# Kernel tuning notes

Measured on AMD Instinct MI355X. Metric: run time of the kernel, lower is better.

## Reference

```python
import jax, jax.numpy as jnp
import numpy as np

COMMITMENT_COST = 0.25
K, D = 1024, 64          # num_embeddings, embedding_dim
B, T = 32, 4096          # batch, tokens per batch element


def setup_inputs() -> dict:
    key = jax.random.key(0)
    k1, k2 = jax.random.split(key)
    inputs = jax.random.normal(k1, (B, T, D), dtype=jnp.float32)
    # xavier_uniform over [K, D]: bound = sqrt(6/(K+D))
    bound = float(np.sqrt(6.0 / (K + D)))
    embedding = jax.random.uniform(k2, (K, D), dtype=jnp.float32,
                                   minval=-bound, maxval=bound)
    return {"inputs": inputs, "embedding": embedding}


def reference(inputs, embedding):
    input_shape = inputs.shape
    flat = inputs.reshape(-1, embedding.shape[1])            # [N, D]
    input_sq = jnp.sum(flat ** 2, axis=1, keepdims=True)     # [N, 1]
    embed_sq = jnp.sum(embedding ** 2, axis=1)               # [K]
    dot = flat @ embedding.T                                 # [N, K]
    distances = input_sq + embed_sq - 2.0 * dot              # [N, K]
    idx = jnp.argmin(distances, axis=1)                      # [N]
    quant = embedding[idx]                                   # [N, D]
    q_latent_loss = jnp.mean((quant - jax.lax.stop_gradient(flat)) ** 2)
    e_latent_loss = jnp.mean((jax.lax.stop_gradient(quant) - flat) ** 2)
    loss = q_latent_loss + COMMITMENT_COST * e_latent_loss
    # straight-through estimator
    quant_st = flat + jax.lax.stop_gradient(quant - flat)
    quant_st = quant_st.reshape(input_shape)
    encoding_indices = idx.reshape(input_shape[0], -1)
    return quant_st, loss, encoding_indices
```

## Files before the change

### kernel.cpp

```cpp
#include <hip/hip_runtime.h>


#define KC 1024
#define DD 64
#define NTOK (32 * 4096)
#define QUANT_ELEMS ((size_t)NTOK * DD)
#define LOSS_OFF QUANT_ELEMS
#define IDX_OFF (QUANT_ELEMS + 1)

#define WS_E2 0
#define WS_BFRAG_F 2048

#define MAIN_BLOCKS (NTOK / 128)

typedef _Float16 f16x8 __attribute__((ext_vector_type(8)));
typedef float f32x4 __attribute__((ext_vector_type(4)));

__device__ __forceinline__ unsigned int sortable_bits(float f) {
  unsigned int b = __float_as_uint(f);
  return b ^ (unsigned int)(((int)b >> 31) | 0x80000000);
}

__device__ __forceinline__ float unsortable_bits(unsigned int u) {
  unsigned int fb = (u & 0x80000000u) ? (u ^ 0x80000000u) : ~u;
  return __uint_as_float(fb);
}

__device__ __forceinline__ float row_sumsq_np8(const float* p) {
  float r[8];
#pragma unroll
  for (int j = 0; j < 8; ++j) r[j] = p[j] * p[j];
#pragma unroll
  for (int i = 1; i < 8; ++i)
#pragma unroll
    for (int j = 0; j < 8; ++j) {
      float v = p[i * 8 + j];
      r[j] += v * v;
    }
  return ((r[0] + r[1]) + (r[2] + r[3])) + ((r[4] + r[5]) + (r[6] + r[7]));
}

__global__ void vq_setup(const float* __restrict__ emb,
                         float* __restrict__ ws,
                         float* __restrict__ out) {
  const int b = blockIdx.x;
  const int tid = threadIdx.x;
  if (b < 64) {
    const int nt = b;
    const int f = tid >> 6;
    const int lane = tid & 63;
    const int plane = f >> 1, ks = f & 1;
    const int n = nt * 16 + (lane & 15);
    const int kb = ks * 32 + ((lane >> 4) & 3) * 8;
    const float* ep = emb + (size_t)n * DD + kb;
    f16x8 o;
#pragma unroll
    for (int j = 0; j < 8; ++j) {
      float v = ep[j];
      _Float16 h = (_Float16)v;
      o[j] = (plane == 0) ? h : (_Float16)(v - (float)h);
    }
    ((f16x8*)(ws + WS_BFRAG_F))[(nt * 4 + f) * 64 + lane] = o;
  } else {
    const int k = (b - 64) * 256 + tid;
    ws[WS_E2 + k] = row_sumsq_np8(emb + (size_t)k * DD);
    if (b == 64 && tid == 0) out[LOSS_OFF] = 0.0f;
  }
}

__launch_bounds__(256, 2)
__global__ void vq_main(const float* __restrict__ x_in,
                        const float* __restrict__ emb,
                        const float* __restrict__ ws_ro,
                        float* __restrict__ out) {
  const int tid = threadIdx.x;
  const int wave = tid >> 6, lane = tid & 63;
  const int quad = lane >> 4, l16 = lane & 15;
  const int blockTok = blockIdx.x * 128;
  const int tokBase = blockTok + wave * 32;

  __shared__ float E2s[KC];
  __shared__ float x2s[128];
  __shared__ float wsum[4];

#pragma unroll
  for (int i = 0; i < 4; ++i)
    E2s[i * 256 + tid] = ws_ro[WS_E2 + i * 256 + tid];
  if (tid < 128)
    x2s[tid] = row_sumsq_np8(x_in + (size_t)(blockTok + tid) * DD);

  f16x8 ah[2][2], al[2][2];
#pragma unroll
  for (int ms = 0; ms < 2; ++ms) {
    const float* xr = x_in + (size_t)(tokBase + ms * 16 + l16) * DD;
#pragma unroll
    for (int ks = 0; ks < 2; ++ks) {
      const float4* p4 = (const float4*)(xr + ks * 32 + quad * 8);
      float4 v0 = p4[0], v1 = p4[1];
      float vv[8] = {v0.x, v0.y, v0.z, v0.w, v1.x, v1.y, v1.z, v1.w};
#pragma unroll
      for (int j = 0; j < 8; ++j) {
        _Float16 h = (_Float16)vv[j];
        ah[ms][ks][j] = h;
        al[ms][ks][j] = (_Float16)(vv[j] - (float)h);
      }
    }
  }

  float best[2][4];
  int bidx[2][4];
#pragma unroll
  for (int ms = 0; ms < 2; ++ms)
#pragma unroll
    for (int r = 0; r < 4; ++r) { best[ms][r] = 3.402823466e38f; bidx[ms][r] = 0; }

  __syncthreads();

  float x2v[2][4];
#pragma unroll
  for (int ms = 0; ms < 2; ++ms)
#pragma unroll
    for (int r = 0; r < 4; ++r)
      x2v[ms][r] = x2s[wave * 32 + ms * 16 + quad * 4 + r];

  const f16x8* bws = (const f16x8*)(ws_ro + WS_BFRAG_F);

  auto compute = [&](int nt, const f16x8 (&bf)[4]) {
    const int ncur = nt * 16 + l16;
    const float e2v = E2s[ncur];
    f32x4 acc[2];
#pragma unroll
    for (int ms = 0; ms < 2; ++ms) acc[ms] = (f32x4){0.f, 0.f, 0.f, 0.f};
    __builtin_amdgcn_s_setprio(1);
#pragma unroll
    for (int ms = 0; ms < 2; ++ms)
      acc[ms] = __builtin_amdgcn_mfma_f32_16x16x32_f16(ah[ms][0], bf[0], acc[ms], 0, 0, 0);
#pragma unroll
    for (int ms = 0; ms < 2; ++ms)
      acc[ms] = __builtin_amdgcn_mfma_f32_16x16x32_f16(ah[ms][1], bf[1], acc[ms], 0, 0, 0);
#pragma unroll
    for (int ms = 0; ms < 2; ++ms)
      acc[ms] = __builtin_amdgcn_mfma_f32_16x16x32_f16(al[ms][0], bf[0], acc[ms], 0, 0, 0);
#pragma unroll
    for (int ms = 0; ms < 2; ++ms)
      acc[ms] = __builtin_amdgcn_mfma_f32_16x16x32_f16(al[ms][1], bf[1], acc[ms], 0, 0, 0);
#pragma unroll
    for (int ms = 0; ms < 2; ++ms)
      acc[ms] = __builtin_amdgcn_mfma_f32_16x16x32_f16(ah[ms][0], bf[2], acc[ms], 0, 0, 0);
#pragma unroll
    for (int ms = 0; ms < 2; ++ms)
      acc[ms] = __builtin_amdgcn_mfma_f32_16x16x32_f16(ah[ms][1], bf[3], acc[ms], 0, 0, 0);
    __builtin_amdgcn_s_setprio(0);
#pragma unroll
    for (int ms = 0; ms < 2; ++ms)
#pragma unroll
      for (int r = 0; r < 4; ++r) {
        float s = __builtin_fmaf(-2.0f, acc[ms][r], x2v[ms][r] + e2v);
        if (s < best[ms][r]) { best[ms][r] = s; bidx[ms][r] = ncur; }
      }
  };

  f16x8 bA[4], bB[4];
#pragma unroll
  for (int i = 0; i < 4; ++i) bA[i] = bws[i * 64 + lane];

  for (int nt = 0; nt < 64; nt += 2) {
#pragma unroll
    for (int i = 0; i < 4; ++i) bB[i] = bws[((nt + 1) * 4 + i) * 64 + lane];
    compute(nt, bA);
    if (nt + 2 < 64) {
#pragma unroll
      for (int i = 0; i < 4; ++i) bA[i] = bws[((nt + 2) * 4 + i) * 64 + lane];
    }
    compute(nt + 1, bB);
  }

  unsigned long long key[2][4];
#pragma unroll
  for (int ms = 0; ms < 2; ++ms)
#pragma unroll
    for (int r = 0; r < 4; ++r) {
      unsigned long long k =
          ((unsigned long long)sortable_bits(best[ms][r]) << 32) |
          (unsigned int)bidx[ms][r];
#pragma unroll
      for (int m = 1; m < 16; m <<= 1) {
        unsigned long long o = __shfl_xor(k, m);
        k = o < k ? o : k;
      }
      key[ms][r] = k;
    }

  float qsum = 0.0f;
#pragma unroll
  for (int ms = 0; ms < 2; ++ms)
#pragma unroll
    for (int r = 0; r < 4; ++r) {
      const int token = tokBase + ms * 16 + quad * 4 + r;
      const int widx = (int)(unsigned int)key[ms][r];
      if (l16 == 0) out[IDX_OFF + (size_t)token] = (float)widx;
      const float4 v = ((const float4*)(emb + (size_t)widx * DD))[l16];
      ((float4*)(out + (size_t)token * DD))[l16] = v;
      qsum += unsortable_bits((unsigned int)(key[ms][r] >> 32));
    }

  float tot = __shfl(qsum, 0) + __shfl(qsum, 16) +
              __shfl(qsum, 32) + __shfl(qsum, 48);
  if (lane == 0) wsum[wave] = tot;
  __syncthreads();
  if (tid == 0) {
    const float scale = 1.25f / (float)QUANT_ELEMS;
    atomicAdd(&out[LOSS_OFF], ((wsum[0] + wsum[1]) + (wsum[2] + wsum[3])) * scale);
  }
}

extern "C" void kernel_launch(void* const* d_in, const int* in_sizes, int n_in,
                              void* d_out, int out_size, void* d_ws, size_t ws_size,
                              hipStream_t stream) {
  const float* x = (const float*)d_in[0];
  const float* emb = (const float*)d_in[1];
  float* out = (float*)d_out;
  float* ws = (float*)d_ws;

  vq_setup<<<68, 256, 0, stream>>>(emb, ws, out);
  vq_main<<<MAIN_BLOCKS, 256, 0, stream>>>(x, emb, ws, out);
}
```

Measured before the change: 136.4 us.

## Switch distance GEMM to 32x32x16 MFMA tiles with reorganized fragments

```diff
diff --git a/kernel.cpp b/kernel.cpp
--- a/kernel.cpp
+++ b/kernel.cpp
@@ -14,7 +14,9 @@
 #define MAIN_BLOCKS (NTOK / 128)
 
 typedef _Float16 f16x8 __attribute__((ext_vector_type(8)));
-typedef float f32x4 __attribute__((ext_vector_type(4)));
+typedef float f32x16 __attribute__((ext_vector_type(16)));
+
+#define MFMA32 __builtin_amdgcn_mfma_f32_32x32x16_f16
 
 __device__ __forceinline__ unsigned int sortable_bits(float f) {
   unsigned int b = __float_as_uint(f);
@@ -45,167 +47,153 @@
                          float* __restrict__ out) {
   const int b = blockIdx.x;
   const int tid = threadIdx.x;
-  if (b < 64) {
-    const int nt = b;
-    const int f = tid >> 6;
+  if (b < 32) {
+    const int T = b;
+    const int q = tid >> 6;
     const int lane = tid & 63;
-    const int plane = f >> 1, ks = f & 1;
-    const int n = nt * 16 + (lane & 15);
-    const int kb = ks * 32 + ((lane >> 4) & 3) * 8;
-    const float* ep = emb + (size_t)n * DD + kb;
-    f16x8 o;
+    const int code = T * 32 + (lane & 31);
+    const int d0 = q * 16 + (lane >> 5) * 8;
+    const float* ep = emb + (size_t)code * DD + d0;
+    f16x8 oh, ol;
 #pragma unroll
     for (int j = 0; j < 8; ++j) {
       float v = ep[j];
-      _Float16 h = (_Float16)v;
-      o[j] = (plane == 0) ? h : (_Float16)(v - (float)h);
-    }
-    ((f16x8*)(ws + WS_BFRAG_F))[(nt * 4 + f) * 64 + lane] = o;
+      _Float16 hv = (_Float16)v;
+      oh[j] = hv;
+      ol[j] = (_Float16)(v - (float)hv);
+    }
+    f16x8* dst = (f16x8*)(ws + WS_BFRAG_F);
+    dst[(T * 8 + q) * 64 + lane] = oh;
+    dst[(T * 8 + 4 + q) * 64 + lane] = ol;
   } else {
-    const int k = (b - 64) * 256 + tid;
+    const int k = (b - 32) * 256 + tid;
     ws[WS_E2 + k] = row_sumsq_np8(emb + (size_t)k * DD);
-    if (b == 64 && tid == 0) out[LOSS_OFF] = 0.0f;
-  }
-}
-
-__launch_bounds__(256, 2)
+    if (b == 32 && tid == 0) out[LOSS_OFF] = 0.0f;
+  }
+}
+
+__launch_bounds__(256, 1)
 __global__ void vq_main(const float* __restrict__ x_in,
                         const float* __restrict__ emb,
                         const float* __restrict__ ws_ro,
                         float* __restrict__ out) {
   const int tid = threadIdx.x;
   const int wave = tid >> 6, lane = tid & 63;
-  const int quad = lane >> 4, l16 = lane & 15;
-  const int blockTok = blockIdx.x * 128;
-  const int tokBase = blockTok + wave * 32;
-
-  __shared__ float E2s[KC];
-  __shared__ float x2s[128];
+  const int c31 = lane & 31, h = lane >> 5;
+  const int tokBase = blockIdx.x * 128 + wave * 32;
+
   __shared__ float wsum[4];
 
-#pragma unroll
-  for (int i = 0; i < 4; ++i)
-    E2s[i * 256 + tid] = ws_ro[WS_E2 + i * 256 + tid];
-  if (tid < 128)
-    x2s[tid] = row_sumsq_np8(x_in + (size_t)(blockTok + tid) * DD);
-
-  f16x8 ah[2][2], al[2][2];
-#pragma unroll
-  for (int ms = 0; ms < 2; ++ms) {
-    const float* xr = x_in + (size_t)(tokBase + ms * 16 + l16) * DD;
-#pragma unroll
-    for (int ks = 0; ks < 2; ++ks) {
-      const float4* p4 = (const float4*)(xr + ks * 32 + quad * 8);
-      float4 v0 = p4[0], v1 = p4[1];
+  const float x2own =
+      row_sumsq_np8(x_in + (size_t)(tokBase + c31) * DD);
+  float x2v[16];
+#pragma unroll
+  for (int r = 0; r < 16; ++r)
+    x2v[r] = __shfl(x2own, (r & 3) + 8 * (r >> 2) + 4 * h);
+
+  f16x8 ah[4], al[4];
+  {
+    const float* xr = x_in + (size_t)(tokBase + c31) * DD + h * 8;
+#pragma unroll
+    for (int q = 0; q < 4; ++q) {
+      const float4 v0 = *(const float4*)(xr + q * 16);
+      const float4 v1 = *(const float4*)(xr + q * 16 + 4);
       float vv[8] = {v0.x, v0.y, v0.z, v0.w, v1.x, v1.y, v1.z, v1.w};
 #pragma unroll
       for (int j = 0; j < 8; ++j) {
-        _Float16 h = (_Float16)vv[j];
-        ah[ms][ks][j] = h;
-        al[ms][ks][j] = (_Float16)(vv[j] - (float)h);
+        _Float16 hv = (_Float16)vv[j];
+        ah[q][j] = hv;
+        al[q][j] = (_Float16)(vv[j] - (float)hv);
       }
     }
   }
 
-  float best[2][4];
-  int bidx[2][4];
-#pragma unroll
-  for (int ms = 0; ms < 2; ++ms)
-#pragma unroll
-    for (int r = 0; r < 4; ++r) { best[ms][r] = 3.402823466e38f; bidx[ms][r] = 0; }
-
-  __syncthreads();
-
-  float x2v[2][4];
-#pragma unroll
-  for (int ms = 0; ms < 2; ++ms)
-#pragma unroll
-    for (int r = 0; r < 4; ++r)
-      x2v[ms][r] = x2s[wave * 32 + ms * 16 + quad * 4 + r];
-
-  const f16x8* bws = (const f16x8*)(ws_ro + WS_BFRAG_F);
-
-  auto compute = [&](int nt, const f16x8 (&bf)[4]) {
-    const int ncur = nt * 16 + l16;
-    const float e2v = E2s[ncur];
-    f32x4 acc[2];
-#pragma unroll
-    for (int ms = 0; ms < 2; ++ms) acc[ms] = (f32x4){0.f, 0.f, 0.f, 0.f};
-    __builtin_amdgcn_s_setprio(1);
-#pragma unroll
-    for (int ms = 0; ms < 2; ++ms)
-      acc[ms] = __builtin_amdgcn_mfma_f32_16x16x32_f16(ah[ms][0], bf[0], acc[ms], 0, 0, 0);
-#pragma unroll
-    for (int ms = 0; ms < 2; ++ms)
-      acc[ms] = __builtin_amdgcn_mfma_f32_16x16x32_f16(ah[ms][1], bf[1], acc[ms], 0, 0, 0);
-#pragma unroll
-    for (int ms = 0; ms < 2; ++ms)
-      acc[ms] = __builtin_amdgcn_mfma_f32_16x16x32_f16(al[ms][0], bf[0], acc[ms], 0, 0, 0);
-#pragma unroll
-    for (int ms = 0; ms < 2; ++ms)
-      acc[ms] = __builtin_amdgcn_mfma_f32_16x16x32_f16(al[ms][1], bf[1], acc[ms], 0, 0, 0);
-#pragma unroll
-    for (int ms = 0; ms < 2; ++ms)
-      acc[ms] = __builtin_amdgcn_mfma_f32_16x16x32_f16(ah[ms][0], bf[2], acc[ms], 0, 0, 0);
-#pragma unroll
-    for (int ms = 0; ms < 2; ++ms)
-      acc[ms] = __builtin_amdgcn_mfma_f32_16x16x32_f16(ah[ms][1], bf[3], acc[ms], 0, 0, 0);
-    __builtin_amdgcn_s_setprio(0);
-#pragma unroll
-    for (int ms = 0; ms < 2; ++ms)
-#pragma unroll
-      for (int r = 0; r < 4; ++r) {
-        float s = __builtin_fmaf(-2.0f, acc[ms][r], x2v[ms][r] + e2v);
-        if (s < best[ms][r]) { best[ms][r] = s; bidx[ms][r] = ncur; }
-      }
-  };
-
-  f16x8 bA[4], bB[4];
-#pragma unroll
-  for (int i = 0; i < 4; ++i) bA[i] = bws[i * 64 + lane];
-
-  for (int nt = 0; nt < 64; nt += 2) {
-#pragma unroll
-    for (int i = 0; i < 4; ++i) bB[i] = bws[((nt + 1) * 4 + i) * 64 + lane];
-    compute(nt, bA);
-    if (nt + 2 < 64) {
-#pragma unroll
-      for (int i = 0; i < 4; ++i) bA[i] = bws[((nt + 2) * 4 + i) * 64 + lane];
-    }
-    compute(nt + 1, bB);
-  }
-
-  unsigned long long key[2][4];
-#pragma unroll
-  for (int ms = 0; ms < 2; ++ms)
-#pragma unroll
-    for (int r = 0; r < 4; ++r) {
-      unsigned long long k =
-          ((unsigned long long)sortable_bits(best[ms][r]) << 32) |
-          (unsigned int)bidx[ms][r];
-#pragma unroll
-      for (int m = 1; m < 16; m <<= 1) {
-        unsigned long long o = __shfl_xor(k, m);
-        k = o < k ? o : k;
-      }
-      key[ms][r] = k;
-    }
+  float best[16];
+  int bidx[16];
+#pragma unroll
+  for (int r = 0; r < 16; ++r) { best[r] = 3.402823466e38f; bidx[r] = 0; }
+
+  const f16x8* bws2 = (const f16x8*)(ws_ro + WS_BFRAG_F);
+  const float* e2p = ws_ro + WS_E2 + c31;
+
+  f16x8 BH[4], BL[4];
+#pragma unroll
+  for (int q = 0; q < 4; ++q) BH[q] = bws2[(0 * 8 + q) * 64 + lane];
+#pragma unroll
+  for (int q = 0; q < 4; ++q) BL[q] = bws2[(0 * 8 + 4 + q) * 64 + lane];
+  float e2v = e2p[0];
+
+#pragma unroll 2
+  for (int T = 0; T < 31; ++T) {
+    f32x16 acc = (f32x16){0.f, 0.f, 0.f, 0.f, 0.f, 0.f, 0.f, 0.f,
+                          0.f, 0.f, 0.f, 0.f, 0.f, 0.f, 0.f, 0.f};
+#pragma unroll
+    for (int q = 0; q < 4; ++q) acc = MFMA32(ah[q], BH[q], acc, 0, 0, 0);
+#pragma unroll
+    for (int q = 0; q < 4; ++q) acc = MFMA32(al[q], BH[q], acc, 0, 0, 0);
+#pragma unroll
+    for (int q = 0; q < 4; ++q) BH[q] = bws2[((T + 1) * 8 + q) * 64 + lane];
+    const float e2n = e2p[(T + 1) * 32];
+#pragma unroll
+    for (int q = 0; q < 4; ++q) acc = MFMA32(ah[q], BL[q], acc, 0, 0, 0);
+#pragma unroll
+    for (int q = 0; q < 4; ++q)
+      BL[q] = bws2[((T + 1) * 8 + 4 + q) * 64 + lane];
+    const int ncur = T * 32 + c31;
+#pragma unroll
+    for (int r = 0; r < 16; ++r) {
+      float s = __builtin_fmaf(-2.0f, acc[r], x2v[r] + e2v);
+      if (s < best[r]) { best[r] = s; bidx[r] = ncur; }
+    }
+    e2v = e2n;
+  }
+  {
+    f32x16 acc = (f32x16){0.f, 0.f, 0.f, 0.f, 0.f, 0.f, 0.f, 0.f,
+                          0.f, 0.f, 0.f, 0.f, 0.f, 0.f, 0.f, 0.f};
+#pragma unroll
+    for (int q = 0; q < 4; ++q) acc = MFMA32(ah[q], BH[q], acc, 0, 0, 0);
+#pragma unroll
+    for (int q = 0; q < 4; ++q) acc = MFMA32(al[q], BH[q], acc, 0, 0, 0);
+#pragma unroll
+    for (int q = 0; q < 4; ++q) acc = MFMA32(ah[q], BL[q], acc, 0, 0, 0);
+    const int ncur = 31 * 32 + c31;
+#pragma unroll
+    for (int r = 0; r < 16; ++r) {
+      float s = __builtin_fmaf(-2.0f, acc[r], x2v[r] + e2v);
+      if (s < best[r]) { best[r] = s; bidx[r] = ncur; }
+    }
+  }
+
+  unsigned long long key[16];
+#pragma unroll
+  for (int r = 0; r < 16; ++r) {
+    unsigned long long k =
+        ((unsigned long long)sortable_bits(best[r]) << 32) |
+        (unsigned int)bidx[r];
+#pragma unroll
+    for (int m = 1; m < 32; m <<= 1) {
+      unsigned long long o = __shfl_xor(k, m);
+      k = o < k ? o : k;
+    }
+    key[r] = k;
+  }
 
   float qsum = 0.0f;
 #pragma unroll
-  for (int ms = 0; ms < 2; ++ms)
-#pragma unroll
-    for (int r = 0; r < 4; ++r) {
-      const int token = tokBase + ms * 16 + quad * 4 + r;
-      const int widx = (int)(unsigned int)key[ms][r];
-      if (l16 == 0) out[IDX_OFF + (size_t)token] = (float)widx;
-      const float4 v = ((const float4*)(emb + (size_t)widx * DD))[l16];
-      ((float4*)(out + (size_t)token * DD))[l16] = v;
-      qsum += unsortable_bits((unsigned int)(key[ms][r] >> 32));
-    }
-
-  float tot = __shfl(qsum, 0) + __shfl(qsum, 16) +
-              __shfl(qsum, 32) + __shfl(qsum, 48);
+  for (int r = 0; r < 16; ++r) {
+    const int token = tokBase + (r & 3) + 8 * (r >> 2) + 4 * h;
+    const int widx = (int)(unsigned int)key[r];
+    if (c31 == 0) {
+      out[IDX_OFF + (size_t)token] = (float)widx;
+      qsum += unsortable_bits((unsigned int)(key[r] >> 32));
+    }
+    if (c31 < 16) {
+      const float4 v = ((const float4*)(emb + (size_t)widx * DD))[c31];
+      ((float4*)(out + (size_t)token * DD))[c31] = v;
+    }
+  }
+
+  float tot = __shfl(qsum, 0) + __shfl(qsum, 32);
   if (lane == 0) wsum[wave] = tot;
   __syncthreads();
   if (tid == 0) {
@@ -222,6 +210,6 @@
   float* out = (float*)d_out;
   float* ws = (float*)d_ws;
 
-  vq_setup<<<68, 256, 0, stream>>>(emb, ws, out);
+  vq_setup<<<36, 256, 0, stream>>>(emb, ws, out);
   vq_main<<<MAIN_BLOCKS, 256, 0, stream>>>(x, emb, ws, out);
 }
```

New measurement: 156.1 us. 1.14x slower.
